# Performance work log

Measured on AMD Instinct MI355X. Metric: run time of the kernel, lower is better.

The kernel has to match this reference:

```python
import jax, jax.numpy as jnp
import numpy as np

IN_F = 2
DIM_H = 64
DT = 0.02          # step_size
INTENSITY = 40.0   # Poisson rate multiplier
RATE = jnp.array([10.0, 1.0], dtype=jnp.float32)  # Gamma rates per feature


def _xavier(key, fan_in, fan_out):
    lim = float(np.sqrt(6.0 / (fan_in + fan_out)))
    return jax.random.uniform(key, (fan_in, fan_out), minval=-lim, maxval=lim, dtype=jnp.float32)


def setup_inputs() -> dict:
    key = jax.random.key(0)
    k0, k1, k2 = jax.random.split(key, 3)
    Nsim, steps = 100000, 200
    z0 = jax.random.normal(k0, (Nsim, IN_F), dtype=jnp.float32)
    W1 = _xavier(k1, IN_F, DIM_H)
    b1 = jnp.zeros((DIM_H,), dtype=jnp.float32)
    W2 = _xavier(k2, DIM_H, IN_F)
    b2 = jnp.zeros((IN_F,), dtype=jnp.float32)
    diffusion = jnp.float32(1.0)
    return {"z0": z0, "W1": W1, "b1": b1, "W2": W2, "b2": b2,
            "diffusion": diffusion, "Nsim": Nsim, "steps": steps}


def _drift(x, W1, b1, W2, b2):
    # MLP: Linear(2,64) -> tanh -> Linear(64,2)
    h = jnp.tanh(x @ W1 + b1)
    return h @ W2 + b2


def reference(z0, W1, b1, W2, b2, diffusion, Nsim, steps):
    sqrt_dt = jnp.float32(np.sqrt(DT))
    n = z0.shape[0]

    def step(state, key):
        kp, kn, kg = jax.random.split(key, 3)
        # Poisson(intensity*dt) jump counts, shape [N,1]
        pois = jax.random.poisson(kp, INTENSITY * DT, (n, 1)).astype(jnp.float32)
        a = jnp.broadcast_to(pois, (n, IN_F))  # Gamma concentration per feature
        # Gamma(conc=pois, rate=RATE); conc==0 -> sample is exactly 0
        g = jax.random.gamma(kg, jnp.maximum(a, 1.0), dtype=jnp.float32) / RATE
        jump = jnp.where(a > 0, g, 0.0)
        noise = jax.random.normal(kn, (n, IN_F), dtype=jnp.float32)
        new_state = (state
                     + _drift(state, W1, b1, W2, b2) * DT
                     + diffusion * sqrt_dt * noise
                     + jump)
        return new_state, new_state

    keys = jax.random.split(jax.random.key(42), steps)
    _, path = jax.lax.scan(step, z0, keys)            # [steps, N, F]
    path = jnp.concatenate([z0[None], path], axis=0)   # [steps+1, N, F]
    return jnp.transpose(path, (1, 0, 2))              # [N, steps+1, F]
```

## Files before the change

### kernel.cpp

```cpp
#include <hip/hip_runtime.h>
#include <cstdint>
#include <cmath>

#define DEVINL __device__ __forceinline__

struct U2 { uint32_t a, b; };
typedef float v2f __attribute__((ext_vector_type(2)));

DEVINL uint32_t rotl32(uint32_t x, uint32_t r){ return (x << r) | (x >> (32u - r)); }

DEVINL U2 tf(uint32_t k0, uint32_t k1, uint32_t x0, uint32_t x1){
  const uint32_t k2 = k0 ^ k1 ^ 0x1BD11BDAu;
  x0 += k0; x1 += k1;
#define TFR(r) { x0 += x1; x1 = rotl32(x1,(r)); x1 ^= x0; }
  TFR(13) TFR(15) TFR(26) TFR(6)  x0 += k1; x1 += k2 + 1u;
  TFR(17) TFR(29) TFR(16) TFR(24) x0 += k2; x1 += k0 + 2u;
  TFR(13) TFR(15) TFR(26) TFR(6)  x0 += k0; x1 += k1 + 3u;
  TFR(17) TFR(29) TFR(16) TFR(24) x0 += k1; x1 += k2 + 4u;
  TFR(13) TFR(15) TFR(26) TFR(6)  x0 += k2; x1 += k0 + 5u;
#undef TFR
  U2 r; r.a = x0; r.b = x1; return r;
}

DEVINL uint32_t pbits(uint32_t k0, uint32_t k1, uint32_t idx){
  U2 r = tf(k0, k1, 0u, idx);
  return r.a ^ r.b;
}

DEVINL float u01(uint32_t bits){
  return __uint_as_float((bits >> 9) | 0x3F800000u) - 1.0f;
}

DEVINL float xla_logf(float xin){
  float xf = fmaxf(__uint_as_float(0x00800000u), xin);
  uint32_t ib = __float_as_uint(xf);
  float e = (float)((int)(ib >> 23) - 126);
  float x = __uint_as_float((ib & 0x807fffffu) | 0x3f000000u);
  bool m = x < 0.707106781186547524f;
  float t = m ? x : 0.0f;
  x = __fsub_rn(x, 1.0f);
  if (m) e = __fsub_rn(e, 1.0f);
  x = __fadd_rn(x, t);
  float z = __fmul_rn(x, x);
  float y = 7.0376836292e-2f;
  y = fmaf(y, x, -1.1514610310e-1f);
  y = fmaf(y, x,  1.1676998740e-1f);
  y = fmaf(y, x, -1.2420140846e-1f);
  y = fmaf(y, x,  1.4249322787e-1f);
  y = fmaf(y, x, -1.6668057665e-1f);
  y = fmaf(y, x,  2.0000714765e-1f);
  y = fmaf(y, x, -2.4999993993e-1f);
  y = fmaf(y, x,  3.3333331174e-1f);
  y = __fmul_rn(y, x);
  y = __fmul_rn(y, z);
  y = fmaf(e, -2.12194440e-4f, y);
  y = fmaf(z, -0.5f, y);
  x = __fadd_rn(x, y);
  x = fmaf(e, 0.693359375f, x);
  if (xin == 0.0f) x = __uint_as_float(0xff800000u);
  return x;
}

DEVINL float xla_log1pf(float v){
  float av = fabsf(v);
  if (av < 1e-4f) return __fmul_rn(__fadd_rn(__fmul_rn(-0.5f, v), 1.0f), v);
  return xla_logf(__fadd_rn(v, 1.0f));
}

DEVINL float erfinv32(float x){
  float xx = __fmul_rn(x, x);
  float w = -xla_log1pf(-xx);
  float p;
  if (w < 5.0f){
    float ww = __fsub_rn(w, 2.5f);
    p = 2.81022636e-08f;
    p = __fadd_rn( 3.43273939e-07f, __fmul_rn(p, ww));
    p = __fadd_rn(-3.5233877e-06f,  __fmul_rn(p, ww));
    p = __fadd_rn(-4.39150654e-06f, __fmul_rn(p, ww));
    p = __fadd_rn( 0.00021858087f,  __fmul_rn(p, ww));
    p = __fadd_rn(-0.00125372503f,  __fmul_rn(p, ww));
    p = __fadd_rn(-0.00417768164f,  __fmul_rn(p, ww));
    p = __fadd_rn( 0.246640727f,    __fmul_rn(p, ww));
    p = __fadd_rn( 1.50140941f,     __fmul_rn(p, ww));
  } else {
    float ww = __fsub_rn(sqrtf(w), 3.0f);
    p = -0.000200214257f;
    p = __fadd_rn( 0.000100950558f, __fmul_rn(p, ww));
    p = __fadd_rn( 0.00134934322f,  __fmul_rn(p, ww));
    p = __fadd_rn(-0.00367342844f,  __fmul_rn(p, ww));
    p = __fadd_rn( 0.00573950773f,  __fmul_rn(p, ww));
    p = __fadd_rn(-0.0076224613f,   __fmul_rn(p, ww));
    p = __fadd_rn( 0.00943887047f,  __fmul_rn(p, ww));
    p = __fadd_rn( 1.00167406f,     __fmul_rn(p, ww));
    p = __fadd_rn( 2.83297682f,     __fmul_rn(p, ww));
  }
  return __fmul_rn(p, x);
}

#define SQRT2F (__uint_as_float(0x3FB504F3u))
#define NLOF   (__uint_as_float(0xBF7FFFFFu))
#define SQDTF  ((float)0.14142135623730951)

DEVINL float normal_from_bits(uint32_t bits){
  float ff = u01(bits);
  float u = __fadd_rn(__fmul_rn(ff, 2.0f), NLOF);
  u = fmaxf(NLOF, u);
  return __fmul_rn(SQRT2F, erfinv32(u));
}

DEVINL float fast_tanh(float x){
  float ax = fabsf(x);
  float e = __expf(-2.0f * ax);
  float r = (1.0f - e) * __builtin_amdgcn_rcpf(1.0f + e);
  return __builtin_copysignf(r, x);
}

DEVINL v2f f2fma(v2f a, v2f b, v2f c){ return __builtin_elementwise_fma(a, b, c); }

DEVINL bool gamma_attempt(uint32_t K0, uint32_t K1, float d, float c, float& out){
  U2 xk = tf(K0, K1, 0u, 1u);
  U2 Uk = tf(K0, K1, 0u, 2u);
  float xx, v;
  for (;;) {
    U2 sub = tf(xk.a, xk.b, 0u, 1u);
    xx = normal_from_bits(pbits(sub.a, sub.b, 0u));
    v = __fadd_rn(1.0f, __fmul_rn(xx, c));
    if (v > 0.0f) break;
    xk = tf(xk.a, xk.b, 0u, 0u);
  }
  float X = __fmul_rn(xx, xx);
  float V = __fmul_rn(__fmul_rn(v, v), v);
  float U = u01(pbits(Uk.a, Uk.b, 0u));
  float sq = __fsub_rn(1.0f, __fmul_rn(0.0331f, __fmul_rn(X, X)));
  if (U < sq) { out = __fmul_rn(d, V); return true; }
  float lnU = xla_logf(U);
  float lnV = xla_logf(V);
  float rhs = __fadd_rn(__fmul_rn(X, 0.5f),
                        __fmul_rn(d, __fadd_rn(__fsub_rn(1.0f, V), lnV)));
  if (lnU < rhs) { out = __fmul_rn(d, V); return true; }
  return false;
}

DEVINL float gamma_fromK(uint32_t K0, uint32_t K1, float alpha){
  const float d = __fsub_rn(alpha, (1.0f/3.0f));
  const float c = (1.0f/3.0f) / sqrtf(d);
  for (;;) {
    float s;
    if (gamma_attempt(K0, K1, d, c, s)) return s;
    U2 K = tf(K0, K1, 0u, 0u);
    K0 = K.a; K1 = K.b;
  }
}

DEVINL float gamma_one(uint32_t gk0, uint32_t gk1, float alpha){
  U2 K = tf(gk0, gk1, 0u, 0u);
  return gamma_fromK(K.a, K.b, alpha);
}

#define NPK 24
#define WSTRIDE (4 + 2*NPK)
#define KEYOFF 8
#define JOFF   16384

__global__ void setup_kernel(uint32_t* __restrict__ ws, int steps){
  int t = blockIdx.x * blockDim.x + threadIdx.x;
  if (t >= steps) return;
  U2 kt = tf(0u, 42u, 0u, (uint32_t)t);
  U2 kp = tf(kt.a, kt.b, 0u, 0u);
  U2 kn = tf(kt.a, kt.b, 0u, 1u);
  U2 kg = tf(kt.a, kt.b, 0u, 2u);
  uint32_t* p = ws + KEYOFF + (size_t)t * WSTRIDE;
  p[0] = kn.a; p[1] = kn.b;
  p[2] = kg.a; p[3] = kg.b;
  uint32_t r0 = kp.a, r1 = kp.b;
  for (int i = 0; i < NPK; ++i) {
    U2 sub = tf(r0, r1, 0u, 1u);
    U2 rn  = tf(r0, r1, 0u, 0u);
    p[4 + 2*i] = sub.a; p[5 + 2*i] = sub.b;
    r0 = rn.a; r1 = rn.b;
  }
}

#define PEL 4
__global__ __launch_bounds__(64) void pois_kernel(
    uint32_t* __restrict__ ws, const float* __restrict__ diffp,
    int N, int steps, uint32_t POFF, uint32_t COFF)
{
  const int lane = threadIdx.x;
  const int t = blockIdx.y;
  const int base = blockIdx.x * (64 * PEL);
  const uint32_t* __restrict__ p = ws + KEYOFF + (size_t)t * WSTRIDE;
  const float coef = __fmul_rn(diffp[0], SQDTF);

  int poisv[PEL];
  #pragma unroll
  for (int j = 0; j < PEL; ++j) poisv[j] = -1;

  int cur = 0;
  int e = base + lane;
  float lp = 0.0f; int k = 0;
  bool done = (e >= N);

  #pragma unroll 1
  for (int guard = 0; guard < PEL * NPK + PEL + 1; ++guard) {
    if (!__any(!done)) break;
    if (!done) {
      if (!(lp > -0.8f)) {
        poisv[cur] = k - 1;
        cur++;
        lp = 0.0f; k = 0;
        int ne = base + cur * 64 + lane;
        if (cur >= PEL || ne >= N) done = true;
        else e = ne;
      }
    }
    if (!done) {
      uint32_t bits = pbits(p[4 + 2*k], p[5 + 2*k], (uint32_t)e);
      lp = __fadd_rn(lp, xla_logf(u01(bits)));
      k++;
      if (k >= NPK) lp = -1.0f;
    }
  }

  float* jarr = (float*)(ws + JOFF);
  uint8_t* pb = (uint8_t*)ws + (size_t)POFF * 4u + (size_t)t * (size_t)N;
  const uint32_t kn0 = p[0], kn1 = p[1];
  int mycnt = 0;
  #pragma unroll
  for (int j = 0; j < PEL; ++j) {
    int ej = base + j * 64 + lane;
    if (ej < N) {
      pb[ej] = (uint8_t)poisv[j];
      float nf0 = normal_from_bits(pbits(kn0, kn1, 2u*(uint32_t)ej));
      float nf1 = normal_from_bits(pbits(kn0, kn1, 2u*(uint32_t)ej + 1u));
      size_t jb = (size_t)t * (size_t)(2*N) + 2u * (uint32_t)ej;
      jarr[jb]     = __fmul_rn(coef, nf0);
      jarr[jb + 1] = __fmul_rn(coef, nf1);
      if (poisv[j] > 0) mycnt++;
    }
  }
  int c = mycnt;
  #pragma unroll
  for (int off = 32; off > 0; off >>= 1) c += __shfl_xor(c, off, 64);
  if (lane == 0)
    ws[COFF + (size_t)t * gridDim.x + blockIdx.x] = (uint32_t)c;
}

__global__ __launch_bounds__(256) void prefix_kernel(
    uint32_t* __restrict__ ws, uint32_t COFF, uint32_t BOFF, int NB, int outIdx)
{
  __shared__ uint32_t ssum[256];
  int i = threadIdx.x;
  int chunk = (NB + 255) >> 8;
  int lo = i * chunk, hi = lo + chunk; if (hi > NB) hi = NB;
  uint32_t s = 0;
  for (int j = lo; j < hi; ++j) s += ws[COFF + j];
  ssum[i] = s;
  __syncthreads();
  if (i == 0) {
    uint32_t run = 0;
    for (int k = 0; k < 256; ++k) { uint32_t c = ssum[k]; ssum[k] = run; run += c; }
    ws[outIdx] = run;
  }
  __syncthreads();
  uint32_t base = ssum[i];
  for (int j = lo; j < hi; ++j) { ws[BOFF + j] = base; base += ws[COFF + j]; }
}

__global__ __launch_bounds__(256) void scatter_kernel(
    uint32_t* __restrict__ ws, int N, int steps,
    uint32_t POFF, uint32_t BOFF, uint32_t WOFF, uint32_t CAP)
{
  __shared__ uint32_t cnts[4];
  int e = blockIdx.x * 256 + threadIdx.x;
  int t = blockIdx.y;
  bool act = e < N;
  uint32_t pv = 0;
  if (act) pv = ((const uint8_t*)ws)[(size_t)POFF*4u + (size_t)t*(size_t)N + (size_t)e];
  uint64_t b = __ballot(pv > 0);
  int lane = threadIdx.x & 63, w = threadIdx.x >> 6;
  if (lane == 0) cnts[w] = (uint32_t)__popcll(b);
  __syncthreads();
  uint32_t bid = (uint32_t)blockIdx.y * gridDim.x + blockIdx.x;
  uint32_t wb = ws[BOFF + bid];
  for (int w2 = 0; w2 < w; ++w2) wb += cnts[w2];
  if (pv > 0) {
    uint32_t rank = (uint32_t)__popcll(b & ((1ull << lane) - 1ull));
    uint32_t idx = wb + rank;
    if (idx < CAP)
      ws[WOFF + idx] = ((uint32_t)t << 23) | ((uint32_t)e << 6) | pv;
  }
}

__global__ __launch_bounds__(256) void gamma_pass1(
    uint32_t* __restrict__ ws, int N,
    uint32_t WOFF, uint32_t CAP, uint32_t FOFF, uint32_t COFF)
{
  __shared__ uint32_t cnts[4];
  uint32_t total = ws[0]; if (total > CAP) total = CAP;
  uint32_t j = blockIdx.x * 256u + threadIdx.x;
  uint32_t fb = 0;
  if (j < total) {
    uint32_t ent = ws[WOFF + j];
    uint32_t t = ent >> 23, e = (ent >> 6) & 0x1FFFFu, pv = ent & 0x3Fu;
    const uint32_t* __restrict__ p = ws + KEYOFF + (size_t)t * WSTRIDE;
    uint32_t kg0 = p[2], kg1 = p[3];
    float alpha = (float)pv;
    const float d = __fsub_rn(alpha, (1.0f/3.0f));
    const float c = (1.0f/3.0f) / sqrtf(d);
    float add0 = 0.0f, add1 = 0.0f;
    {
      U2 gk = tf(kg0, kg1, 0u, 2u*e);
      U2 K  = tf(gk.a, gk.b, 0u, 0u);
      float s;
      if (gamma_attempt(K.a, K.b, d, c, s)) add0 = s / 10.0f; else fb |= 1u;
    }
    {
      U2 gk = tf(kg0, kg1, 0u, 2u*e + 1u);
      U2 K  = tf(gk.a, gk.b, 0u, 0u);
      float s;
      if (gamma_attempt(K.a, K.b, d, c, s)) add1 = s; else fb |= 2u;
    }
    float* jarr = (float*)(ws + JOFF);
    float2* slot = (float2*)&jarr[(size_t)t * (size_t)(2*N) + (size_t)(2u*e)];
    float2 v = *slot;
    v.x = __fadd_rn(v.x, add0);
    v.y = __fadd_rn(v.y, add1);
    *slot = v;
  }
  if (j < CAP) ((uint8_t*)ws)[(size_t)FOFF*4u + j] = (uint8_t)fb;
  uint64_t b = __ballot(fb != 0u);
  int lane = threadIdx.x & 63, w = threadIdx.x >> 6;
  if (lane == 0) cnts[w] = (uint32_t)__popcll(b);
  __syncthreads();
  if (threadIdx.x == 0)
    ws[COFF + blockIdx.x] = cnts[0] + cnts[1] + cnts[2] + cnts[3];
}

__global__ __launch_bounds__(256) void retry_scatter(
    uint32_t* __restrict__ ws, uint32_t FOFF, uint32_t BOFF,
    uint32_t WOFF, uint32_t CAP)
{
  __shared__ uint32_t cnts[4];
  uint32_t totalA = ws[0]; if (totalA > CAP) totalA = CAP;
  uint32_t spare = CAP - totalA;
  uint32_t j = blockIdx.x * 256u + threadIdx.x;
  uint32_t fb = 0;
  if (j < CAP) fb = ((const uint8_t*)ws)[(size_t)FOFF*4u + j];
  uint64_t b = __ballot(fb != 0u);
  int lane = threadIdx.x & 63, w = threadIdx.x >> 6;
  if (lane == 0) cnts[w] = (uint32_t)__popcll(b);
  __syncthreads();
  uint32_t wb = ws[BOFF + blockIdx.x];
  for (int w2 = 0; w2 < w; ++w2) wb += cnts[w2];
  if (fb != 0u) {
    uint32_t rank = (uint32_t)__popcll(b & ((1ull << lane) - 1ull));
    uint32_t idx = wb + rank;
    if (idx < spare) ws[WOFF + totalA + idx] = (j << 2) | fb;
  }
}

__global__ __launch_bounds__(256) void retry_exec(
    uint32_t* __restrict__ ws, int N, uint32_t WOFF, uint32_t CAP, uint32_t RMAX)
{
  uint32_t totalA = ws[0]; if (totalA > CAP) totalA = CAP;
  uint32_t spare = CAP - totalA;
  uint32_t rtot = ws[1];
  if (rtot > spare) rtot = spare;
  if (rtot > RMAX) rtot = RMAX;
  uint32_t i = blockIdx.x * 256u + threadIdx.x;
  if (i >= rtot) return;
  uint32_t rec = ws[WOFF + totalA + i];
  uint32_t j = rec >> 2, fb = rec & 3u;
  uint32_t ent = ws[WOFF + j];
  uint32_t t = ent >> 23, e = (ent >> 6) & 0x1FFFFu, pv = ent & 0x3Fu;
  const uint32_t* __restrict__ p = ws + KEYOFF + (size_t)t * WSTRIDE;
  float alpha = (float)pv;
  float* jarr = (float*)(ws + JOFF);
  size_t jb = (size_t)t * (size_t)(2*N) + (size_t)(2u*e);
  if (fb & 1u) {
    U2 gk = tf(p[2], p[3], 0u, 2u*e);
    U2 K  = tf(gk.a, gk.b, 0u, 0u);
    K = tf(K.a, K.b, 0u, 0u);
    float s = gamma_fromK(K.a, K.b, alpha) / 10.0f;
    jarr[jb] = __fadd_rn(jarr[jb], s);
  }
  if (fb & 2u) {
    U2 gk = tf(p[2], p[3], 0u, 2u*e + 1u);
    U2 K  = tf(gk.a, gk.b, 0u, 0u);
    K = tf(K.a, K.b, 0u, 0u);
    float s = gamma_fromK(K.a, K.b, alpha);
    jarr[jb + 1] = __fadd_rn(jarr[jb + 1], s);
  }
}

__global__ __launch_bounds__(256) void jump_kernel(
    uint32_t* __restrict__ ws, const float* __restrict__ diffp, int N, int steps)
{
  int e = blockIdx.x * 256 + threadIdx.x;
  int t = blockIdx.y;
  if (e >= N) return;
  const uint32_t* __restrict__ p = ws + KEYOFF + (size_t)t * WSTRIDE;
  const uint32_t ue = (uint32_t)e;
  const float coef = __fmul_rn(diffp[0], SQDTF);
  float lp = 0.0f; int k = 0;
  #pragma unroll 1
  for (int i = 0; i < NPK; ++i) {
    if (!(lp > -0.8f)) break;
    k++;
    uint32_t bits = pbits(p[4 + 2*i], p[5 + 2*i], ue);
    lp = __fadd_rn(lp, xla_logf(u01(bits)));
  }
  int pois = k - 1;
  float nf0 = normal_from_bits(pbits(p[0], p[1], 2u*ue));
  float nf1 = normal_from_bits(pbits(p[0], p[1], 2u*ue + 1u));
  float j0 = __fmul_rn(coef, nf0), j1 = __fmul_rn(coef, nf1);
  if (pois > 0) {
    uint32_t kg0 = p[2], kg1 = p[3];
    float alpha = (float)pois;
    U2 gk0 = tf(kg0, kg1, 0u, 2u*ue);
    j0 = __fadd_rn(j0, gamma_one(gk0.a, gk0.b, alpha) / 10.0f);
    U2 gk1 = tf(kg0, kg1, 0u, 2u*ue + 1u);
    j1 = __fadd_rn(j1, gamma_one(gk1.a, gk1.b, alpha));
  }
  float* jarr = (float*)(ws + JOFF);
  size_t jbase = (size_t)t * (size_t)(2*N) + (size_t)(2*e);
  jarr[jbase] = j0; jarr[jbase + 1] = j1;
}

#define IBLK 256
__global__ __launch_bounds__(IBLK) void integrate_kernel(
    const float* __restrict__ z0, const float* __restrict__ W1,
    const float* __restrict__ b1, const float* __restrict__ W2,
    const float* __restrict__ b2, const float* __restrict__ diffp,
    const uint32_t* __restrict__ ws, float* __restrict__ out,
    int N, int steps)
{
  __shared__ float smem[322];
  for (int k = threadIdx.x; k < 322; k += IBLK) {
    float v;
    if (k < 128)      v = W1[k];
    else if (k < 192) v = b1[k - 128];
    else if (k < 320) v = W2[k - 192];
    else              v = b2[k - 320];
    smem[k] = v;
  }
  __syncthreads();
  const float* sW1 = smem;
  const float* sb1 = smem + 128;
  const float* sW2 = smem + 192;
  const float* sb2 = smem + 320;

  int tid = blockIdx.x * IBLK + threadIdx.x;
  const int e = tid >> 3;
  const int s = tid & 7;
  if (e >= N) return;

  float2 xv = *(const float2*)&z0[2*e];
  float x0 = xv.x, x1 = xv.y;
  const size_t orow = (size_t)(steps + 1) * 2u;
  float* op = out + (size_t)e * orow;
  if (s == 0) *(float2*)&op[0] = xv;

  const float DTf  = 0.02f;
  const int   hbase = s << 3;
  const float2* __restrict__ jarr2 = (const float2*)(ws + JOFF);
  const float b20 = sb2[0], b21 = sb2[1];

  for (int t = 0; t < steps; ++t) {
    float2 S = jarr2[(size_t)t * (size_t)N + (size_t)e];

    v2f xv0 = (v2f){x0, x0};
    v2f xv1 = (v2f){x1, x1};
    v2f accA = (v2f){0.0f, 0.0f};
    v2f accB = (v2f){0.0f, 0.0f};
    #pragma unroll
    for (int j = 0; j < 2; ++j) {
      {
        int h = hbase + 2*j;
        v2f pre = f2fma(xv0, *(const v2f*)&sW1[h],
                  f2fma(xv1, *(const v2f*)&sW1[64 + h], *(const v2f*)&sb1[h]));
        float hv0 = fast_tanh(pre.x);
        float hv1 = fast_tanh(pre.y);
        accA = f2fma((v2f){hv0, hv0}, *(const v2f*)&sW2[2*h], accA);
        accA = f2fma((v2f){hv1, hv1}, *(const v2f*)&sW2[2*h + 2], accA);
      }
      {
        int h = hbase + 4 + 2*j;
        v2f pre = f2fma(xv0, *(const v2f*)&sW1[h],
                  f2fma(xv1, *(const v2f*)&sW1[64 + h], *(const v2f*)&sb1[h]));
        float hv0 = fast_tanh(pre.x);
        float hv1 = fast_tanh(pre.y);
        accB = f2fma((v2f){hv0, hv0}, *(const v2f*)&sW2[2*h], accB);
        accB = f2fma((v2f){hv1, hv1}, *(const v2f*)&sW2[2*h + 2], accB);
      }
    }
    v2f acc = accA + accB;
    float q0 = acc.x, q1 = acc.y;
    q0 = q0 + __shfl_xor(q0, 1, 64);
    q1 = q1 + __shfl_xor(q1, 1, 64);
    q0 = q0 + __shfl_xor(q0, 2, 64);
    q1 = q1 + __shfl_xor(q1, 2, 64);
    q0 = q0 + __shfl_xor(q0, 4, 64);
    q1 = q1 + __shfl_xor(q1, 4, 64);
    float dr0 = b20 + q0;
    float dr1 = b21 + q1;

    x0 = __fadd_rn(__fadd_rn(x0, __fmul_rn(dr0, DTf)), S.x);
    x1 = __fadd_rn(__fadd_rn(x1, __fmul_rn(dr1, DTf)), S.y);
    if (s == 0) {
      float2 o; o.x = x0; o.y = x1;
      *(float2*)&op[(size_t)(t + 1) * 2u] = o;
    }
  }
}

__global__ __launch_bounds__(64) void sim_fallback_kernel(
    const float* __restrict__ z0, const float* __restrict__ W1,
    const float* __restrict__ b1, const float* __restrict__ W2,
    const float* __restrict__ b2, const float* __restrict__ diffp,
    const uint32_t* __restrict__ ws, float* __restrict__ out,
    int N, int steps)
{
  __shared__ float smem[322];
  for (int k = threadIdx.x; k < 322; k += 64) {
    float v;
    if (k < 128)      v = W1[k];
    else if (k < 192) v = b1[k - 128];
    else if (k < 320) v = W2[k - 192];
    else              v = b2[k - 320];
    smem[k] = v;
  }
  __syncthreads();
  const float* sW1 = smem;
  const float* sb1 = smem + 128;
  const float* sW2 = smem + 192;
  const float* sb2 = smem + 320;

  int tid = blockIdx.x * 64 + threadIdx.x;
  if (tid >= 2 * N) return;
  const int e = tid >> 1;
  const int f = tid & 1;
  const uint32_t ue   = (uint32_t)e;
  const uint32_t utid = (uint32_t)tid;

  float x = z0[tid];
  const size_t obase = (size_t)e * (size_t)(steps + 1) * 2u + (size_t)f;
  out[obase] = x;

  const float DTf  = 0.02f;
  const float coef = __fmul_rn(diffp[0], SQDTF);
  const int   hbase = f << 5;

  for (int t = 0; t < steps; ++t) {
    const uint32_t* __restrict__ p = ws + KEYOFF + (size_t)t * WSTRIDE;
    int pois;
    {
      float lp = 0.0f;
      pois = NPK - 1;
      #pragma unroll 1
      for (int m = 0; m < NPK/2; ++m) {
        int i0 = 2*m + f;
        uint32_t bits = pbits(p[4 + 2*i0], p[5 + 2*i0], ue);
        float lmine = xla_logf(u01(bits));
        float lother = __shfl_xor(lmine, 1, 64);
        float la = (f == 0) ? lmine : lother;
        float lb = (f == 0) ? lother : lmine;
        float s1 = __fadd_rn(lp, la);
        float s2 = __fadd_rn(s1, lb);
        if (!(s1 > -0.8f)) { pois = 2*m; break; }
        if (!(s2 > -0.8f)) { pois = 2*m + 1; break; }
        lp = s2;
      }
    }
    float nf = normal_from_bits(pbits(p[0], p[1], utid));
    float jump = 0.0f;
    if (pois > 0) {
      U2 gk = tf(p[2], p[3], 0u, utid);
      float s = gamma_one(gk.a, gk.b, (float)pois);
      jump = (f == 0) ? (s / 10.0f) : s;
    }
    float xo = __shfl_xor(x, 1, 64);
    float xf0 = (f == 0) ? x : xo;
    float xf1 = (f == 0) ? xo : x;
    float p0 = 0.0f, p1 = 0.0f;
    #pragma unroll
    for (int i = 0; i < 32; ++i) {
      int h = hbase + i;
      float hv = fast_tanh(fmaf(xf0, sW1[h], fmaf(xf1, sW1[64 + h], sb1[h])));
      p0 = fmaf(hv, sW2[2*h],     p0);
      p1 = fmaf(hv, sW2[2*h + 1], p1);
    }
    float q0 = p0 + __shfl_xor(p0, 1, 64);
    float q1 = p1 + __shfl_xor(p1, 1, 64);
    float dr = sb2[f] + ((f == 0) ? q0 : q1);
    x = __fadd_rn(__fadd_rn(__fadd_rn(x, __fmul_rn(dr, DTf)),
                            __fmul_rn(coef, nf)), jump);
    out[obase + (size_t)(t + 1) * 2u] = x;
  }
}

extern "C" void kernel_launch(void* const* d_in, const int* in_sizes, int n_in,
                              void* d_out, int out_size, void* d_ws, size_t ws_size,
                              hipStream_t stream) {
  const float* z0  = (const float*)d_in[0];
  const float* W1  = (const float*)d_in[1];
  const float* b1  = (const float*)d_in[2];
  const float* W2  = (const float*)d_in[3];
  const float* b2  = (const float*)d_in[4];
  const float* dif = (const float*)d_in[5];
  int N = in_sizes[0] / 2;
  int steps = out_size / (N * 2) - 1;
  uint32_t* ws = (uint32_t*)d_ws;
  int total = 2 * N;

  hipLaunchKernelGGL(setup_kernel, dim3((steps + 255) / 256), dim3(256), 0, stream,
                     ws, steps);

  size_t JSZ = (size_t)2 * (size_t)N * (size_t)steps;
  size_t PSZ = ((size_t)N * (size_t)steps + 3u) / 4u;
  int    NBX = (N + 255) / 256;
  size_t NB  = (size_t)NBX * (size_t)steps;
  size_t CAP = ((size_t)N * (size_t)steps * 11u) / 16u;
  size_t POFFs = (size_t)JOFF + JSZ;
  size_t COFFs = POFFs + PSZ;
  size_t BOFFs = COFFs + NB;
  size_t WOFFs = BOFFs + NB;
  size_t need0 = (WOFFs + CAP) * 4u;
  size_t need1 = ((size_t)JOFF + JSZ) * 4u;
  int    NB2 = (int)((CAP + 255u) / 256u);
  bool pk = (N < (1 << 17)) && (steps < (1 << 9)) && (steps <= 314) &&
            ((size_t)NB2 <= NB) && (WOFFs + CAP < 0xFFFFFFFFull);

  int total8 = 8 * N;

  if (pk && ws_size >= need0) {
    hipLaunchKernelGGL(pois_kernel, dim3(NBX, steps), dim3(64), 0, stream,
                       ws, dif, N, steps, (uint32_t)POFFs, (uint32_t)COFFs);
    hipLaunchKernelGGL(prefix_kernel, dim3(1), dim3(256), 0, stream,
                       ws, (uint32_t)COFFs, (uint32_t)BOFFs, (int)NB, 0);
    hipLaunchKernelGGL(scatter_kernel, dim3(NBX, steps), dim3(256), 0, stream,
                       ws, N, steps, (uint32_t)POFFs, (uint32_t)BOFFs,
                       (uint32_t)WOFFs, (uint32_t)CAP);
    hipLaunchKernelGGL(gamma_pass1, dim3(NB2), dim3(256), 0, stream,
                       ws, N, (uint32_t)WOFFs, (uint32_t)CAP,
                       (uint32_t)POFFs, (uint32_t)COFFs);
    hipLaunchKernelGGL(prefix_kernel, dim3(1), dim3(256), 0, stream,
                       ws, (uint32_t)COFFs, (uint32_t)BOFFs, NB2, 1);
    hipLaunchKernelGGL(retry_scatter, dim3(NB2), dim3(256), 0, stream,
                       ws, (uint32_t)POFFs, (uint32_t)BOFFs,
                       (uint32_t)WOFFs, (uint32_t)CAP);
    uint32_t RMAX = (uint32_t)(((CAP / 4u) + 255u) / 256u) * 256u;
    hipLaunchKernelGGL(retry_exec, dim3(RMAX / 256u), dim3(256), 0, stream,
                       ws, N, (uint32_t)WOFFs, (uint32_t)CAP, RMAX);
    hipLaunchKernelGGL(integrate_kernel, dim3((total8 + IBLK - 1) / IBLK), dim3(IBLK),
                       0, stream, z0, W1, b1, W2, b2, dif, ws, (float*)d_out, N, steps);
  } else if (steps <= 314 && ws_size >= need1) {
    hipLaunchKernelGGL(jump_kernel, dim3((N + 255) / 256, steps), dim3(256), 0, stream,
                       ws, dif, N, steps);
    hipLaunchKernelGGL(integrate_kernel, dim3((total8 + IBLK - 1) / IBLK), dim3(IBLK),
                       0, stream, z0, W1, b1, W2, b2, dif, ws, (float*)d_out, N, steps);
  } else {
    hipLaunchKernelGGL(sim_fallback_kernel, dim3((total + 63) / 64), dim3(64), 0, stream,
                       z0, W1, b1, W2, b2, dif, ws, (float*)d_out, N, steps);
  }
}
```

Baseline: 1.473 ms.

## Split Poisson sampling into a two-draw fast pass and compacted retry pass

Replaces the per-wave Poisson loop, which ran a divergent wave-synchronous loop over four elements per lane, with a 256-thread kernel that draws only the first two uniforms per element and writes counts 0/1 directly. Elements still above the threshold after two draws are compacted via ballot into per-block record slots, and a separate retry kernel continues their sampling. The goal is to remove divergence and serialized looping for the common case where Poisson(0.8) is 0 or 1. It adds a kernel launch and a fixed per-block slot limit (RSLOT) that could overflow, plus packed counts read by prefix_kernel through a 16-bit mask.

```diff
diff --git a/kernel.cpp b/kernel.cpp
--- a/kernel.cpp
+++ b/kernel.cpp
@@ -161,6 +161,7 @@
 #define WSTRIDE (4 + 2*NPK)
 #define KEYOFF 8
 #define JOFF   16384
+#define RSLOT 128
 
 __global__ void setup_kernel(uint32_t* __restrict__ ws, int steps){
   int t = blockIdx.x * blockDim.x + threadIdx.x;
@@ -181,80 +182,101 @@
   }
 }
 
-#define PEL 4
-__global__ __launch_bounds__(64) void pois_kernel(
+__global__ __launch_bounds__(256) void pois1_kernel(
     uint32_t* __restrict__ ws, const float* __restrict__ diffp,
-    int N, int steps, uint32_t POFF, uint32_t COFF)
-{
-  const int lane = threadIdx.x;
-  const int t = blockIdx.y;
-  const int base = blockIdx.x * (64 * PEL);
+    int N, int steps, uint32_t POFF, uint32_t COFF, uint32_t WOFF)
+{
+  __shared__ uint32_t gcnts[4], rcnts[4];
+  int e = blockIdx.x * 256 + threadIdx.x;
+  int t = blockIdx.y;
+  bool act = e < N;
   const uint32_t* __restrict__ p = ws + KEYOFF + (size_t)t * WSTRIDE;
   const float coef = __fmul_rn(diffp[0], SQDTF);
 
-  int poisv[PEL];
-  #pragma unroll
-  for (int j = 0; j < PEL; ++j) poisv[j] = -1;
-
-  int cur = 0;
-  int e = base + lane;
-  float lp = 0.0f; int k = 0;
-  bool done = (e >= N);
-
-  #pragma unroll 1
-  for (int guard = 0; guard < PEL * NPK + PEL + 1; ++guard) {
-    if (!__any(!done)) break;
-    if (!done) {
-      if (!(lp > -0.8f)) {
-        poisv[cur] = k - 1;
-        cur++;
-        lp = 0.0f; k = 0;
-        int ne = base + cur * 64 + lane;
-        if (cur >= PEL || ne >= N) done = true;
-        else e = ne;
-      }
-    }
-    if (!done) {
-      uint32_t bits = pbits(p[4 + 2*k], p[5 + 2*k], (uint32_t)e);
+  bool g = false, retry = false;
+  float lp2 = 0.0f;
+  int pois01 = 0;
+  if (act) {
+    const uint32_t ue = (uint32_t)e;
+    float l1 = xla_logf(u01(pbits(p[4], p[5], ue)));
+    float l2 = xla_logf(u01(pbits(p[6], p[7], ue)));
+    float lpa = __fadd_rn(0.0f, l1);
+    g = (lpa > -0.8f);
+    lp2 = __fadd_rn(lpa, l2);
+    retry = g && (lp2 > -0.8f);
+    pois01 = g ? 1 : 0;
+    float nf0 = normal_from_bits(pbits(p[0], p[1], 2u*ue));
+    float nf1 = normal_from_bits(pbits(p[0], p[1], 2u*ue + 1u));
+    float* jarr = (float*)(ws + JOFF);
+    size_t jb = (size_t)t * (size_t)(2*N) + 2u*ue;
+    jarr[jb]     = __fmul_rn(coef, nf0);
+    jarr[jb + 1] = __fmul_rn(coef, nf1);
+    ((uint8_t*)ws)[(size_t)POFF*4u + (size_t)t*(size_t)N + (size_t)e] =
+        (uint8_t)pois01;
+  }
+
+  uint64_t gb = __ballot(g);
+  uint64_t rb = __ballot(retry);
+  int lane = threadIdx.x & 63, w = threadIdx.x >> 6;
+  if (lane == 0) { gcnts[w] = (uint32_t)__popcll(gb); rcnts[w] = (uint32_t)__popcll(rb); }
+  __syncthreads();
+  uint32_t bid = (uint32_t)blockIdx.y * gridDim.x + blockIdx.x;
+  if (retry) {
+    uint32_t base = 0;
+    for (int w2 = 0; w2 < w; ++w2) base += rcnts[w2];
+    uint32_t rank = base + (uint32_t)__popcll(rb & ((1ull << lane) - 1ull));
+    if (rank < RSLOT) {
+      uint32_t* rec = ws + WOFF + (size_t)bid * (2u*RSLOT) + 2u*rank;
+      rec[0] = ((uint32_t)t << 23) | ((uint32_t)e << 6);
+      rec[1] = __float_as_uint(lp2);
+    }
+  }
+  if (threadIdx.x == 0) {
+    uint32_t gc = gcnts[0] + gcnts[1] + gcnts[2] + gcnts[3];
+    uint32_t rc = rcnts[0] + rcnts[1] + rcnts[2] + rcnts[3];
+    ws[COFF + bid] = gc | (rc << 16);
+  }
+}
+
+__global__ __launch_bounds__(64) void pois_retry_kernel(
+    uint32_t* __restrict__ ws, int N, uint32_t POFF, uint32_t COFF, uint32_t WOFF)
+{
+  uint32_t bid = (uint32_t)blockIdx.y * gridDim.x + blockIdx.x;
+  uint32_t cnt = ws[COFF + bid] >> 16;
+  if (cnt > RSLOT) cnt = RSLOT;
+  const int t = blockIdx.y;
+  const uint32_t* __restrict__ p = ws + KEYOFF + (size_t)t * WSTRIDE;
+  uint8_t* pb = (uint8_t*)ws + (size_t)POFF * 4u + (size_t)t * (size_t)N;
+  const uint32_t* base = ws + WOFF + (size_t)bid * (2u*RSLOT);
+  for (uint32_t r = threadIdx.x; r < cnt; r += 64) {
+    uint32_t rec0 = base[2*r];
+    float lp = __uint_as_float(base[2*r + 1]);
+    uint32_t e = (rec0 >> 6) & 0x1FFFFu;
+    int k = 2;
+    #pragma unroll 1
+    while (lp > -0.8f && k < NPK) {
+      uint32_t bits = pbits(p[4 + 2*k], p[5 + 2*k], e);
       lp = __fadd_rn(lp, xla_logf(u01(bits)));
       k++;
-      if (k >= NPK) lp = -1.0f;
-    }
-  }
-
-  float* jarr = (float*)(ws + JOFF);
-  uint8_t* pb = (uint8_t*)ws + (size_t)POFF * 4u + (size_t)t * (size_t)N;
-  const uint32_t kn0 = p[0], kn1 = p[1];
-  int mycnt = 0;
-  #pragma unroll
-  for (int j = 0; j < PEL; ++j) {
-    int ej = base + j * 64 + lane;
-    if (ej < N) {
-      pb[ej] = (uint8_t)poisv[j];
-      float nf0 = normal_from_bits(pbits(kn0, kn1, 2u*(uint32_t)ej));
-      float nf1 = normal_from_bits(pbits(kn0, kn1, 2u*(uint32_t)ej + 1u));
-      size_t jb = (size_t)t * (size_t)(2*N) + 2u * (uint32_t)ej;
-      jarr[jb]     = __fmul_rn(coef, nf0);
-      jarr[jb + 1] = __fmul_rn(coef, nf1);
-      if (poisv[j] > 0) mycnt++;
-    }
-  }
-  int c = mycnt;
-  #pragma unroll
-  for (int off = 32; off > 0; off >>= 1) c += __shfl_xor(c, off, 64);
-  if (lane == 0)
-    ws[COFF + (size_t)t * gridDim.x + blockIdx.x] = (uint32_t)c;
+    }
+    int pois = (lp > -0.8f) ? (NPK - 1) : (k - 1);
+    pb[e] = (uint8_t)pois;
+  }
 }
 
 __global__ __launch_bounds__(256) void prefix_kernel(
-    uint32_t* __restrict__ ws, uint32_t COFF, uint32_t BOFF, int NB, int outIdx)
+    uint32_t* __restrict__ ws, uint32_t COFF, uint32_t BOFF, int NB,
+    int outIdx, int mask16)
 {
   __shared__ uint32_t ssum[256];
   int i = threadIdx.x;
   int chunk = (NB + 255) >> 8;
   int lo = i * chunk, hi = lo + chunk; if (hi > NB) hi = NB;
   uint32_t s = 0;
-  for (int j = lo; j < hi; ++j) s += ws[COFF + j];
+  for (int j = lo; j < hi; ++j) {
+    uint32_t v = ws[COFF + j];
+    s += mask16 ? (v & 0xFFFFu) : v;
+  }
   ssum[i] = s;
   __syncthreads();
   if (i == 0) {
@@ -264,7 +286,11 @@
   }
   __syncthreads();
   uint32_t base = ssum[i];
-  for (int j = lo; j < hi; ++j) { ws[BOFF + j] = base; base += ws[COFF + j]; }
+  for (int j = lo; j < hi; ++j) {
+    ws[BOFF + j] = base;
+    uint32_t v = ws[COFF + j];
+    base += mask16 ? (v & 0xFFFFu) : v;
+  }
 }
 
 __global__ __launch_bounds__(256) void scatter_kernel(
@@ -456,6 +482,7 @@
   const int s = tid & 7;
   if (e >= N) return;
 
+  const int hb = s << 3;
   float2 xv = *(const float2*)&z0[2*e];
   float x0 = xv.x, x1 = xv.y;
   const size_t orow = (size_t)(steps + 1) * 2u;
@@ -463,7 +490,6 @@
   if (s == 0) *(float2*)&op[0] = xv;
 
   const float DTf  = 0.02f;
-  const int   hbase = s << 3;
   const float2* __restrict__ jarr2 = (const float2*)(ws + JOFF);
   const float b20 = sb2[0], b21 = sb2[1];
 
@@ -477,20 +503,18 @@
     #pragma unroll
     for (int j = 0; j < 2; ++j) {
       {
-        int h = hbase + 2*j;
+        int h = hb + 2*j;
         v2f pre = f2fma(xv0, *(const v2f*)&sW1[h],
                   f2fma(xv1, *(const v2f*)&sW1[64 + h], *(const v2f*)&sb1[h]));
-        float hv0 = fast_tanh(pre.x);
-        float hv1 = fast_tanh(pre.y);
+        float hv0 = fast_tanh(pre.x), hv1 = fast_tanh(pre.y);
         accA = f2fma((v2f){hv0, hv0}, *(const v2f*)&sW2[2*h], accA);
         accA = f2fma((v2f){hv1, hv1}, *(const v2f*)&sW2[2*h + 2], accA);
       }
       {
-        int h = hbase + 4 + 2*j;
+        int h = hb + 4 + 2*j;
         v2f pre = f2fma(xv0, *(const v2f*)&sW1[h],
                   f2fma(xv1, *(const v2f*)&sW1[64 + h], *(const v2f*)&sb1[h]));
-        float hv0 = fast_tanh(pre.x);
-        float hv1 = fast_tanh(pre.y);
+        float hv0 = fast_tanh(pre.x), hv1 = fast_tanh(pre.y);
         accB = f2fma((v2f){hv0, hv0}, *(const v2f*)&sW2[2*h], accB);
         accB = f2fma((v2f){hv1, hv1}, *(const v2f*)&sW2[2*h + 2], accB);
       }
@@ -630,15 +654,19 @@
   size_t need1 = ((size_t)JOFF + JSZ) * 4u;
   int    NB2 = (int)((CAP + 255u) / 256u);
   bool pk = (N < (1 << 17)) && (steps < (1 << 9)) && (steps <= 314) &&
-            ((size_t)NB2 <= NB) && (WOFFs + CAP < 0xFFFFFFFFull);
+            ((size_t)NB2 <= NB) && (NB * (2u*RSLOT) <= CAP) &&
+            (WOFFs + CAP < 0xFFFFFFFFull);
 
   int total8 = 8 * N;
 
   if (pk && ws_size >= need0) {
-    hipLaunchKernelGGL(pois_kernel, dim3(NBX, steps), dim3(64), 0, stream,
-                       ws, dif, N, steps, (uint32_t)POFFs, (uint32_t)COFFs);
+    hipLaunchKernelGGL(pois1_kernel, dim3(NBX, steps), dim3(256), 0, stream,
+                       ws, dif, N, steps, (uint32_t)POFFs, (uint32_t)COFFs,
+                       (uint32_t)WOFFs);
+    hipLaunchKernelGGL(pois_retry_kernel, dim3(NBX, steps), dim3(64), 0, stream,
+                       ws, N, (uint32_t)POFFs, (uint32_t)COFFs, (uint32_t)WOFFs);
     hipLaunchKernelGGL(prefix_kernel, dim3(1), dim3(256), 0, stream,
-                       ws, (uint32_t)COFFs, (uint32_t)BOFFs, (int)NB, 0);
+                       ws, (uint32_t)COFFs, (uint32_t)BOFFs, (int)NB, 0, 1);
     hipLaunchKernelGGL(scatter_kernel, dim3(NBX, steps), dim3(256), 0, stream,
                        ws, N, steps, (uint32_t)POFFs, (uint32_t)BOFFs,
                        (uint32_t)WOFFs, (uint32_t)CAP);
@@ -646,7 +674,7 @@
                        ws, N, (uint32_t)WOFFs, (uint32_t)CAP,
                        (uint32_t)POFFs, (uint32_t)COFFs);
     hipLaunchKernelGGL(prefix_kernel, dim3(1), dim3(256), 0, stream,
-                       ws, (uint32_t)COFFs, (uint32_t)BOFFs, NB2, 1);
+                       ws, (uint32_t)COFFs, (uint32_t)BOFFs, NB2, 1, 0);
     hipLaunchKernelGGL(retry_scatter, dim3(NB2), dim3(256), 0, stream,
                        ws, (uint32_t)POFFs, (uint32_t)BOFFs,
                        (uint32_t)WOFFs, (uint32_t)CAP);
```

Result: slower. 1.696 ms (+15.1%).
